# Optimization experiments

Hardware: AMD Instinct MI355X
Metric: run time of the kernel (lower is better)

Reference implementation:

```python
import jax, jax.numpy as jnp
import numpy as np

N = 100000      # nodes_num
H = 256         # n_hid
E = 3200000     # edges (avg degree 32)
OUT = 2         # GATConv out_feats, num_heads = 1
NEG_SLOPE = 0.2 # DGL GATConv default leaky_relu slope


def setup_inputs() -> dict:
    key = jax.random.key(0)
    ks = jax.random.split(key, 8)
    return {
        "input": jax.random.normal(ks[0], (N, H), dtype=jnp.float32),
        "x": jax.random.normal(ks[1], (N, 1), dtype=jnp.float32),  # the torch.randn inside forward, made deterministic
        "degree": jnp.ones((N, 1), dtype=jnp.float32),             # unused by forward, kept for signature fidelity
        "edge_src": jax.random.randint(ks[2], (E,), 0, N, dtype=jnp.int32),
        "edge_dst": jax.random.randint(ks[3], (E,), 0, N, dtype=jnp.int32),
        "W": jax.random.normal(ks[4], (H, OUT), dtype=jnp.float32) * (1.0 / np.sqrt(H)),
        "attn_l": jax.random.normal(ks[5], (OUT,), dtype=jnp.float32),
        "attn_r": jax.random.normal(ks[6], (OUT,), dtype=jnp.float32),
        "bias": jax.random.normal(ks[7], (OUT,), dtype=jnp.float32) * 0.02,
    }


def _gat_conv(feat, edge_src, edge_dst, W, attn_l, attn_r, bias):
    # DGL GATConv, num_heads=1. feat: [N,H] -> [N,OUT]
    z = feat @ W                              # [N, OUT]
    el = z @ attn_l                           # [N] source term
    er = z @ attn_r                           # [N] dest term
    e = jax.nn.leaky_relu(el[edge_src] + er[edge_dst], NEG_SLOPE)  # [E]
    # edge softmax grouped by destination node (numerically stable)
    m = jax.ops.segment_max(e, edge_dst, num_segments=N)           # [N]
    ex = jnp.exp(e - m[edge_dst])                                  # [E]
    denom = jax.ops.segment_sum(ex, edge_dst, num_segments=N)      # [N]
    alpha = ex / denom[edge_dst]                                   # [E]
    out = jax.ops.segment_sum(alpha[:, None] * z[edge_src], edge_dst, num_segments=N)
    return out + bias                         # [N, OUT]


def reference(input, x, degree, edge_src, edge_dst, W, attn_l, attn_r, bias):
    coff = _gat_conv(input, edge_src, edge_dst, W, attn_l, attn_r, bias)  # [N, 2]
    # torch: mean over heads dim (num_heads=1) is identity
    std = jax.nn.relu(coff[:, 0:1])   # [N,1]
    mean = jax.nn.relu(coff[:, 1:2])  # [N,1]
    # y = ones, so y*mean == mean
    return input * jax.nn.sigmoid(x * std + mean)
```

## Files before the change

kernel.cpp:

```cpp
#include <hip/hip_runtime.h>
#include <hip/hip_fp16.h>
#include <math.h>

#define HDIM 256
#define NEG_SLOPE 0.2f


#define BSHIFT 7
#define BMASK 127
#define MAXBKT 1024
#define EPB 6144
#define BINTHREADS 512
#define PROCTHREADS 1024

__device__ __forceinline__ float leaky(float v) {
    return v >= 0.0f ? v : NEG_SLOPE * v;
}

__device__ __forceinline__ unsigned enc_f32(float f) {
    unsigned b = __float_as_uint(f);
    return b ^ ((b >> 31) ? 0xFFFFFFFFu : 0x80000000u);
}
__device__ __forceinline__ float dec_f32(unsigned u) {
    u ^= ((u >> 31) ? 0x80000000u : 0xFFFFFFFFu);
    return __uint_as_float(u);
}

__global__ void k_node(const float* __restrict__ input,
                       const float* __restrict__ W,
                       const float* __restrict__ attn_l,
                       const float* __restrict__ attn_r,
                       float4* __restrict__ nodeinfo,
                       float* __restrict__ el_arr,
                       float* __restrict__ er_arr,
                       int n)
{
    int node = blockIdx.x * 4 + (threadIdx.x >> 6);
    int lane = threadIdx.x & 63;
    if (node >= n) return;

    const float4* inrow = (const float4*)(input + (size_t)node * HDIM);
    float4 v = inrow[lane];
    const float4* Wv = (const float4*)W;
    float4 w0 = Wv[2 * lane];
    float4 w1 = Wv[2 * lane + 1];
    float s0 = v.x * w0.x + v.y * w0.z + v.z * w1.x + v.w * w1.z;
    float s1 = v.x * w0.y + v.y * w0.w + v.z * w1.y + v.w * w1.w;

    #pragma unroll
    for (int off = 32; off > 0; off >>= 1) {
        s0 += __shfl_xor(s0, off);
        s1 += __shfl_xor(s1, off);
    }

    if (lane == 0) {
        float el = s0 * attn_l[0] + s1 * attn_l[1];
        float er = s0 * attn_r[0] + s1 * attn_r[1];
        nodeinfo[node] = make_float4(el, er, s0, s1);
        el_arr[node] = el;
        er_arr[node] = er;
    }
}

__global__ void k_maxel(const float* __restrict__ el, unsigned* __restrict__ M_enc, int n)
{
    float m = -1e30f;
    for (int i = blockIdx.x * blockDim.x + threadIdx.x; i < n;
         i += gridDim.x * blockDim.x)
        m = fmaxf(m, el[i]);
    #pragma unroll
    for (int off = 32; off > 0; off >>= 1)
        m = fmaxf(m, __shfl_xor(m, off));
    __shared__ float s[4];
    int lane = threadIdx.x & 63, w = threadIdx.x >> 6;
    if (lane == 0) s[w] = m;
    __syncthreads();
    if (threadIdx.x == 0) {
        float mm = fmaxf(fmaxf(s[0], s[1]), fmaxf(s[2], s[3]));
        atomicMax(M_enc, enc_f32(mm));
    }
}

__global__ __launch_bounds__(BINTHREADS)
void k_bin(const int* __restrict__ src,
           const int* __restrict__ dst,
           unsigned* __restrict__ cursor,
           unsigned* __restrict__ edgebuf,
           const float4* __restrict__ nodeinfo,
           const float* __restrict__ er_arr,
           const unsigned* __restrict__ M_enc,
           unsigned* __restrict__ num,
           float* __restrict__ denom,
           int e, int nbkt, int cap)
{
    __shared__ unsigned h1[MAXBKT];
    __shared__ unsigned h2[MAXBKT];
    __shared__ unsigned recs[EPB];
    __shared__ unsigned short bkt[EPB];

    for (int t = threadIdx.x; t < nbkt; t += blockDim.x) { h1[t] = 0u; h2[t] = 0u; }
    __syncthreads();

    int lo = blockIdx.x * EPB;
    int cnt = min(EPB, e - lo);

    if (cnt == EPB) {
        const int4* s4 = (const int4*)(src + lo);
        const int4* d4 = (const int4*)(dst + lo);
        #pragma unroll
        for (int k = 0; k < EPB / (4 * BINTHREADS); ++k) {
            int i4 = (int)threadIdx.x + k * BINTHREADS;
            int4 sv = s4[i4];
            int4 dv = d4[i4];
            int i = 4 * i4;
            recs[i + 0] = ((unsigned)sv.x << BSHIFT) | ((unsigned)dv.x & BMASK);
            recs[i + 1] = ((unsigned)sv.y << BSHIFT) | ((unsigned)dv.y & BMASK);
            recs[i + 2] = ((unsigned)sv.z << BSHIFT) | ((unsigned)dv.z & BMASK);
            recs[i + 3] = ((unsigned)sv.w << BSHIFT) | ((unsigned)dv.w & BMASK);
            bkt[i + 0] = (unsigned short)((unsigned)dv.x >> BSHIFT);
            bkt[i + 1] = (unsigned short)((unsigned)dv.y >> BSHIFT);
            bkt[i + 2] = (unsigned short)((unsigned)dv.z >> BSHIFT);
            bkt[i + 3] = (unsigned short)((unsigned)dv.w >> BSHIFT);
            atomicAdd(&h1[(unsigned)dv.x >> BSHIFT], 1u);
            atomicAdd(&h1[(unsigned)dv.y >> BSHIFT], 1u);
            atomicAdd(&h1[(unsigned)dv.z >> BSHIFT], 1u);
            atomicAdd(&h1[(unsigned)dv.w >> BSHIFT], 1u);
        }
    } else {
        for (int i = threadIdx.x; i < cnt; i += blockDim.x) {
            int s = src[lo + i];
            int d = dst[lo + i];
            recs[i] = ((unsigned)s << BSHIFT) | ((unsigned)d & BMASK);
            bkt[i] = (unsigned short)((unsigned)d >> BSHIFT);
            atomicAdd(&h1[(unsigned)d >> BSHIFT], 1u);
        }
    }
    __syncthreads();

    for (int t = threadIdx.x; t < nbkt; t += blockDim.x) {
        unsigned c = h1[t];
        h1[t] = c ? atomicAdd(&cursor[t], c) : 0u;
    }
    __syncthreads();

    for (int i = threadIdx.x; i < cnt; i += blockDim.x) {
        int b = (int)bkt[i];
        unsigned rec = recs[i];
        unsigned r = h1[b] + atomicAdd(&h2[b], 1u);
        if (r < (unsigned)cap) {
            edgebuf[(size_t)b * cap + r] = rec;
        } else {
            int s = (int)(rec >> BSHIFT);
            int d = (b << BSHIFT) | (int)(rec & BMASK);
            float Mel = dec_f32(*M_enc);
            float4 ns = nodeinfo[s];
            float erd = er_arr[d];
            float ex = __expf(leaky(ns.x + erd) - leaky(Mel + erd));
            __half2 h = __floats2half2_rn(ex * ns.z, ex * ns.w);
            unsigned hv = *(unsigned*)&h;
            unsigned* np = num + d;
            asm volatile("global_atomic_pk_add_f16 %0, %1, off"
                         :: "v"(np), "v"(hv) : "memory");
            float* dp = denom + d;
            asm volatile("global_atomic_add_f32 %0, %1, off"
                         :: "v"(dp), "v"(ex) : "memory");
        }
    }
}

__global__ __launch_bounds__(PROCTHREADS)
void k_proc(const unsigned* __restrict__ cursor,
            const unsigned* __restrict__ edgebuf,
            const float4* __restrict__ nodeinfo,
            const float* __restrict__ er_arr,
            const unsigned* __restrict__ M_enc,
            const unsigned* __restrict__ num,
            const float* __restrict__ denom,
            const float* __restrict__ x,
            const float* __restrict__ bias,
            float* __restrict__ g,
            int n, int cap)
{
    __shared__ float sD[128], s0[128], s1[128], ser[128];
    int b = blockIdx.x;
    int dbase = b << BSHIFT;
    int t = threadIdx.x;
    if (t < 128) {
        sD[t] = 0.f; s0[t] = 0.f; s1[t] = 0.f;
        int d = dbase + t;
        ser[t] = (d < n) ? er_arr[d] : 0.f;
    }
    __syncthreads();

    float Mel = dec_f32(*M_enc);
    unsigned cnt = cursor[b];
    if (cnt > (unsigned)cap) cnt = (unsigned)cap;
    const unsigned* buf = edgebuf + (size_t)b * cap;
    const uint4* buf4 = (const uint4*)buf;
    unsigned nvec = cnt >> 2;

    #define PROC1(rec, ns) do {                                        \
        int dl_ = (int)((rec) & BMASK);                                \
        float erd_ = ser[dl_];                                         \
        float ex_ = __expf(leaky((ns).x + erd_) - leaky(Mel + erd_));  \
        atomicAdd(&sD[dl_], ex_);                                      \
        atomicAdd(&s0[dl_], ex_ * (ns).z);                             \
        atomicAdd(&s1[dl_], ex_ * (ns).w);                             \
    } while (0)

    for (unsigned i4 = (unsigned)t; i4 < nvec; i4 += blockDim.x) {
        uint4 ra = buf4[i4];
        float4 na0 = nodeinfo[ra.x >> BSHIFT];
        float4 na1 = nodeinfo[ra.y >> BSHIFT];
        float4 na2 = nodeinfo[ra.z >> BSHIFT];
        float4 na3 = nodeinfo[ra.w >> BSHIFT];
        PROC1(ra.x, na0); PROC1(ra.y, na1); PROC1(ra.z, na2); PROC1(ra.w, na3);
    }
    for (unsigned i = (nvec << 2) + (unsigned)t; i < cnt; i += blockDim.x) {
        unsigned rec = buf[i];
        float4 ns = nodeinfo[rec >> BSHIFT];
        PROC1(rec, ns);
    }
    #undef PROC1
    __syncthreads();

    if (t < 128) {
        int d = dbase + t;
        if (d < n) {
            float D = sD[t] + denom[d];
            __half2 h = *(const __half2*)(num + d);
            float2 f = __half22float2(h);
            float S0 = s0[t] + f.x;
            float S1 = s1[t] + f.y;
            float c0 = bias[0], c1 = bias[1];
            if (D > 0.f) { float inv = 1.0f / D; c0 += S0 * inv; c1 += S1 * inv; }
            float tt = x[d] * fmaxf(c0, 0.f) + fmaxf(c1, 0.f);
            g[d] = 1.0f / (1.0f + __expf(-tt));
        }
    }
}

__global__ void k_edge(const int* __restrict__ src,
                       const int* __restrict__ dst,
                       const float4* __restrict__ nodeinfo,
                       const float* __restrict__ er_arr,
                       const unsigned* __restrict__ M_enc,
                       unsigned* __restrict__ num,
                       float* __restrict__ denom,
                       int e)
{
    int i = blockIdx.x * blockDim.x + threadIdx.x;
    if (i >= e) return;
    float Mel = dec_f32(*M_enc);
    int s = src[i], d = dst[i];
    float4 ns = nodeinfo[s];
    float erd = er_arr[d];
    float ex = __expf(leaky(ns.x + erd) - leaky(Mel + erd));
    __half2 h = __floats2half2_rn(ex * ns.z, ex * ns.w);
    unsigned hv = *(unsigned*)&h;
    unsigned* np = num + d;
    asm volatile("global_atomic_pk_add_f16 %0, %1, off"
                 :: "v"(np), "v"(hv) : "memory");
    float* dp = denom + d;
    asm volatile("global_atomic_add_f32 %0, %1, off"
                 :: "v"(dp), "v"(ex) : "memory");
}

__global__ void k_reduce(const unsigned* __restrict__ num,
                         const float* __restrict__ denom,
                         const float* __restrict__ x,
                         const float* __restrict__ bias,
                         float* __restrict__ g,
                         int n)
{
    int i = blockIdx.x * blockDim.x + threadIdx.x;
    if (i >= n) return;
    float D = denom[i];
    float c0 = bias[0], c1 = bias[1];
    if (D > 0.0f) {
        __half2 h = *(const __half2*)(num + i);
        float2 f = __half22float2(h);
        float inv = 1.0f / D;
        c0 += f.x * inv;
        c1 += f.y * inv;
    }
    float t = x[i] * fmaxf(c0, 0.0f) + fmaxf(c1, 0.0f);
    g[i] = 1.0f / (1.0f + __expf(-t));
}

__global__ void k_final(const float* __restrict__ input,
                        const float* __restrict__ g,
                        float* __restrict__ out,
                        int n)
{
    int node = blockIdx.x * 4 + (threadIdx.x >> 6);
    int lane = threadIdx.x & 63;
    if (node >= n) return;
    float gg = g[node];
    const float4* inrow = (const float4*)(input + (size_t)node * HDIM);
    float4* outrow = (float4*)(out + (size_t)node * HDIM);
    float4 v = inrow[lane];
    outrow[lane] = make_float4(v.x * gg, v.y * gg, v.z * gg, v.w * gg);
}

extern "C" void kernel_launch(void* const* d_in, const int* in_sizes, int n_in,
                              void* d_out, int out_size, void* d_ws, size_t ws_size,
                              hipStream_t stream)
{
    const float* input  = (const float*)d_in[0];
    const float* x      = (const float*)d_in[1];
    const int* esrc     = (const int*)d_in[3];
    const int* edst     = (const int*)d_in[4];
    const float* W      = (const float*)d_in[5];
    const float* attn_l = (const float*)d_in[6];
    const float* attn_r = (const float*)d_in[7];
    const float* bias   = (const float*)d_in[8];
    float* out = (float*)d_out;

    const int n = in_sizes[1];
    const int e = in_sizes[3];

    char* ws = (char*)d_ws;
    unsigned* num      = (unsigned*)ws;
    float*    denom    = (float*)(ws + (size_t)4 * n);
    unsigned* M_enc    = (unsigned*)(ws + (size_t)8 * n);
    unsigned* cursor   = (unsigned*)(ws + (size_t)8 * n + 64);
    size_t    base2    = (size_t)8 * n + 64 + 4 * MAXBKT;
    float4*   nodeinfo = (float4*)(ws + base2);
    float*    el_arr   = (float*)(ws + base2 + (size_t)16 * n);
    float*    er_arr   = (float*)(ws + base2 + (size_t)20 * n);
    float*    g        = (float*)(ws + base2 + (size_t)24 * n);
    unsigned* edgebuf  = (unsigned*)(ws + base2 + (size_t)28 * n);

    const int nbkt  = (n + BMASK) >> BSHIFT;
    const int meanb = (nbkt > 0) ? e / nbkt : 0;
    int cap = meanb + meanb / 4 + 64;
    cap = (cap + 3) & ~3;
    const size_t need_fast = base2 + (size_t)28 * n + 4ull * nbkt * cap;
    const bool fast = (nbkt <= MAXBKT) && (ws_size >= need_fast);

    hipMemsetAsync(ws, 0, (size_t)8 * n + 64 + 4 * MAXBKT, stream);

    dim3 blk(256);
    int nodeBlocks = (n + 3) / 4;
    int flatBlocks = (n + 255) / 256;

    k_node<<<nodeBlocks, blk, 0, stream>>>(input, W, attn_l, attn_r,
                                           nodeinfo, el_arr, er_arr, n);
    k_maxel<<<120, blk, 0, stream>>>(el_arr, M_enc, n);

    if (fast) {
        int binBlocks = (e + EPB - 1) / EPB;
        k_bin<<<binBlocks, dim3(BINTHREADS), 0, stream>>>(
            esrc, edst, cursor, edgebuf, nodeinfo, er_arr, M_enc, num, denom,
            e, nbkt, cap);
        k_proc<<<nbkt, dim3(PROCTHREADS), 0, stream>>>(
            cursor, edgebuf, nodeinfo, er_arr, M_enc,
            num, denom, x, bias, g, n, cap);
    } else {
        int edgeBlocks = (e + 255) / 256;
        k_edge<<<edgeBlocks, blk, 0, stream>>>(esrc, edst, nodeinfo, er_arr, M_enc,
                                               num, denom, e);
        k_reduce<<<flatBlocks, blk, 0, stream>>>(num, denom, x, bias, g, n);
    }

    k_final<<<nodeBlocks, blk, 0, stream>>>(input, g, out, n);
}
```

Measured before the change: 328.6 us.

## Fuse global el max into node kernel and use grid-stride persistent blocks

Folds the separate max-of-el reduction into the node projection kernel, so each block tracks a local max and does one atomicMax, and drops the el_arr buffer and one kernel launch. Both the node kernel and the final scaling kernel now run a fixed grid of persistent blocks that loop over nodes with a wave-stride, in place of one block per four nodes. This cuts launch and block-scheduling overhead and the extra read of el. In exchange, each wave handles several nodes in sequence, which may reduce memory-level parallelism per wave.

```diff
diff --git a/kernel.cpp b/kernel.cpp
--- a/kernel.cpp
+++ b/kernel.cpp
@@ -12,6 +12,7 @@
 #define EPB 6144
 #define BINTHREADS 512
 #define PROCTHREADS 1024
+#define PERSIST_BLOCKS 2048
 
 __device__ __forceinline__ float leaky(float v) {
     return v >= 0.0f ? v : NEG_SLOPE * v;
@@ -26,57 +27,52 @@
     return __uint_as_float(u);
 }
 
-__global__ void k_node(const float* __restrict__ input,
-                       const float* __restrict__ W,
-                       const float* __restrict__ attn_l,
-                       const float* __restrict__ attn_r,
-                       float4* __restrict__ nodeinfo,
-                       float* __restrict__ el_arr,
-                       float* __restrict__ er_arr,
-                       int n)
-{
-    int node = blockIdx.x * 4 + (threadIdx.x >> 6);
+__global__ __launch_bounds__(256)
+void k_node(const float* __restrict__ input,
+            const float* __restrict__ W,
+            const float* __restrict__ attn_l,
+            const float* __restrict__ attn_r,
+            float4* __restrict__ nodeinfo,
+            float* __restrict__ er_arr,
+            unsigned* __restrict__ M_enc,
+            int n)
+{
     int lane = threadIdx.x & 63;
-    if (node >= n) return;
-
-    const float4* inrow = (const float4*)(input + (size_t)node * HDIM);
-    float4 v = inrow[lane];
+    int wid  = threadIdx.x >> 6;
+    int gwave = blockIdx.x * 4 + wid;
+    int nwaves = gridDim.x * 4;
+
     const float4* Wv = (const float4*)W;
     float4 w0 = Wv[2 * lane];
     float4 w1 = Wv[2 * lane + 1];
-    float s0 = v.x * w0.x + v.y * w0.z + v.z * w1.x + v.w * w1.z;
-    float s1 = v.x * w0.y + v.y * w0.w + v.z * w1.y + v.w * w1.w;
-
-    #pragma unroll
-    for (int off = 32; off > 0; off >>= 1) {
-        s0 += __shfl_xor(s0, off);
-        s1 += __shfl_xor(s1, off);
-    }
-
-    if (lane == 0) {
-        float el = s0 * attn_l[0] + s1 * attn_l[1];
-        float er = s0 * attn_r[0] + s1 * attn_r[1];
-        nodeinfo[node] = make_float4(el, er, s0, s1);
-        el_arr[node] = el;
-        er_arr[node] = er;
-    }
-}
-
-__global__ void k_maxel(const float* __restrict__ el, unsigned* __restrict__ M_enc, int n)
-{
-    float m = -1e30f;
-    for (int i = blockIdx.x * blockDim.x + threadIdx.x; i < n;
-         i += gridDim.x * blockDim.x)
-        m = fmaxf(m, el[i]);
-    #pragma unroll
-    for (int off = 32; off > 0; off >>= 1)
-        m = fmaxf(m, __shfl_xor(m, off));
-    __shared__ float s[4];
-    int lane = threadIdx.x & 63, w = threadIdx.x >> 6;
-    if (lane == 0) s[w] = m;
+    float al0 = attn_l[0], al1 = attn_l[1];
+    float ar0 = attn_r[0], ar1 = attn_r[1];
+
+    float lmax = -1e30f;
+    for (int node = gwave; node < n; node += nwaves) {
+        const float4* inrow = (const float4*)(input + (size_t)node * HDIM);
+        float4 v = inrow[lane];
+        float s0 = v.x * w0.x + v.y * w0.z + v.z * w1.x + v.w * w1.z;
+        float s1 = v.x * w0.y + v.y * w0.w + v.z * w1.y + v.w * w1.w;
+        #pragma unroll
+        for (int off = 32; off > 0; off >>= 1) {
+            s0 += __shfl_xor(s0, off);
+            s1 += __shfl_xor(s1, off);
+        }
+        if (lane == 0) {
+            float el = s0 * al0 + s1 * al1;
+            float er = s0 * ar0 + s1 * ar1;
+            nodeinfo[node] = make_float4(el, er, s0, s1);
+            er_arr[node] = er;
+            lmax = fmaxf(lmax, el);
+        }
+    }
+
+    __shared__ float sm[4];
+    if (lane == 0) sm[wid] = lmax;
     __syncthreads();
     if (threadIdx.x == 0) {
-        float mm = fmaxf(fmaxf(s[0], s[1]), fmaxf(s[2], s[3]));
+        float mm = fmaxf(fmaxf(sm[0], sm[1]), fmaxf(sm[2], sm[3]));
         atomicMax(M_enc, enc_f32(mm));
     }
 }
@@ -288,19 +284,24 @@
     g[i] = 1.0f / (1.0f + __expf(-t));
 }
 
-__global__ void k_final(const float* __restrict__ input,
-                        const float* __restrict__ g,
-                        float* __restrict__ out,
-                        int n)
-{
-    int node = blockIdx.x * 4 + (threadIdx.x >> 6);
+__global__ __launch_bounds__(256)
+void k_final(const float* __restrict__ input,
+             const float* __restrict__ g,
+             float* __restrict__ out,
+             int n)
+{
     int lane = threadIdx.x & 63;
-    if (node >= n) return;
-    float gg = g[node];
-    const float4* inrow = (const float4*)(input + (size_t)node * HDIM);
-    float4* outrow = (float4*)(out + (size_t)node * HDIM);
-    float4 v = inrow[lane];
-    outrow[lane] = make_float4(v.x * gg, v.y * gg, v.z * gg, v.w * gg);
+    int wid  = threadIdx.x >> 6;
+    int gwave = blockIdx.x * 4 + wid;
+    int nwaves = gridDim.x * 4;
+
+    for (int node = gwave; node < n; node += nwaves) {
+        float gg = g[node];
+        const float4* inrow = (const float4*)(input + (size_t)node * HDIM);
+        float4* outrow = (float4*)(out + (size_t)node * HDIM);
+        float4 v = inrow[lane];
+        outrow[lane] = make_float4(v.x * gg, v.y * gg, v.z * gg, v.w * gg);
+    }
 }
 
 extern "C" void kernel_launch(void* const* d_in, const int* in_sizes, int n_in,
@@ -327,7 +328,6 @@
     unsigned* cursor   = (unsigned*)(ws + (size_t)8 * n + 64);
     size_t    base2    = (size_t)8 * n + 64 + 4 * MAXBKT;
     float4*   nodeinfo = (float4*)(ws + base2);
-    float*    el_arr   = (float*)(ws + base2 + (size_t)16 * n);
     float*    er_arr   = (float*)(ws + base2 + (size_t)20 * n);
     float*    g        = (float*)(ws + base2 + (size_t)24 * n);
     unsigned* edgebuf  = (unsigned*)(ws + base2 + (size_t)28 * n);
@@ -342,12 +342,11 @@
     hipMemsetAsync(ws, 0, (size_t)8 * n + 64 + 4 * MAXBKT, stream);
 
     dim3 blk(256);
-    int nodeBlocks = (n + 3) / 4;
-    int flatBlocks = (n + 255) / 256;
-
-    k_node<<<nodeBlocks, blk, 0, stream>>>(input, W, attn_l, attn_r,
-                                           nodeinfo, el_arr, er_arr, n);
-    k_maxel<<<120, blk, 0, stream>>>(el_arr, M_enc, n);
+    int persistBlocks = PERSIST_BLOCKS;
+    if (persistBlocks > (n + 3) / 4) persistBlocks = (n + 3) / 4;
+
+    k_node<<<persistBlocks, blk, 0, stream>>>(input, W, attn_l, attn_r,
+                                              nodeinfo, er_arr, M_enc, n);
 
     if (fast) {
         int binBlocks = (e + EPB - 1) / EPB;
@@ -359,10 +358,11 @@
             num, denom, x, bias, g, n, cap);
     } else {
         int edgeBlocks = (e + 255) / 256;
+        int flatBlocks = (n + 255) / 256;
         k_edge<<<edgeBlocks, blk, 0, stream>>>(esrc, edst, nodeinfo, er_arr, M_enc,
                                                num, denom, e);
         k_reduce<<<flatBlocks, blk, 0, stream>>>(num, denom, x, bias, g, n);
     }
 
-    k_final<<<nodeBlocks, blk, 0, stream>>>(input, g, out, n);
-}
+    k_final<<<persistBlocks, blk, 0, stream>>>(input, g, out, n);
+}
```

Result: slower. 354.0 us (+7.7%).
